# Performance work log

Measured on AMD Instinct MI355X. Metric: run time of the kernel, lower is better.

The kernel has to match this reference:

```python
import jax, jax.numpy as jnp
import numpy as np

DIM = 1024
N_HEADS = 16
MLP_DIM = 4096
DEPTH = 6
HEAD_DIM = DIM // N_HEADS
SCALE = DIM ** -0.5  # module uses full dim (self.dim_heads = dim), NOT head_dim
EPS = 1e-5


def setup_inputs() -> dict:
    key = jax.random.key(0)
    ks = jax.random.split(key, 12)
    s = lambda k, shape, fan: jax.random.normal(k, shape, jnp.float32) * (fan ** -0.5)
    return {
        "x": jax.random.normal(ks[0], (8, 1024, DIM), jnp.float32),
        "Wq": s(ks[1], (DIM, DIM), DIM), "bq": jnp.zeros((DIM,), jnp.float32),
        "Wk": s(ks[2], (DIM, DIM), DIM), "bk": jnp.zeros((DIM,), jnp.float32),
        "Wv": s(ks[3], (DIM, DIM), DIM), "bv": jnp.zeros((DIM,), jnp.float32),
        "W1": s(ks[4], (DIM, MLP_DIM), DIM), "b1": jnp.zeros((MLP_DIM,), jnp.float32),
        "W2": s(ks[5], (MLP_DIM, DIM), MLP_DIM), "b2": jnp.zeros((DIM,), jnp.float32),
        "gamma": jnp.ones((DIM,), jnp.float32),
        "beta": jnp.zeros((DIM,), jnp.float32),
    }


def _layernorm(x, gamma, beta):
    mu = jnp.mean(x, axis=-1, keepdims=True)
    var = jnp.mean(jnp.square(x - mu), axis=-1, keepdims=True)
    return (x - mu) * jax.lax.rsqrt(var + EPS) * gamma + beta


def _attention(x, Wq, bq, Wk, bk, Wv, bv):
    b, n, _ = x.shape
    split = lambda t: t.reshape(b, n, N_HEADS, HEAD_DIM).transpose(0, 2, 1, 3)  # b h n d
    q = split(x @ Wq + bq)
    k = split(x @ Wk + bk)
    v = split(x @ Wv + bv)
    logit = jnp.einsum('bhnd,bhmd->bhnm', q, k) * SCALE
    attn = jax.nn.softmax(logit, axis=-1)
    out = jnp.einsum('bhnm,bhmd->bhnd', attn, v)
    return out.transpose(0, 2, 1, 3).reshape(b, n, DIM)


def reference(x, Wq, bq, Wk, bk, Wv, bv, W1, b1, W2, b2, gamma, beta):
    # Same single attention + MLP modules (shared weights) applied `depth` times.
    for _ in range(DEPTH):
        x = _attention(_layernorm(x, gamma, beta), Wq, bq, Wk, bk, Wv, bv) + x
        h = _layernorm(x, gamma, beta)
        x = (jax.nn.gelu(h @ W1 + b1, approximate=False) @ W2 + b2) + x
    return x
```

## Files before the change

### kernel.cpp

```cpp
#include <hip/hip_runtime.h>
#include <cstdint>
#include <cmath>

typedef short bf16x8 __attribute__((ext_vector_type(8)));
typedef float f32x4 __attribute__((ext_vector_type(4)));

#define AS_GLOBAL(p) (const __attribute__((address_space(1))) void*)(p)
#define AS_LDS(p)    (__attribute__((address_space(3))) void*)(p)

#define QSCALE 0.04508422002778f

__device__ inline float b2f(unsigned short u) {
    union { unsigned int i; float f; } c; c.i = ((unsigned int)u) << 16; return c.f;
}
__device__ inline unsigned short f2b(float f) {
    return (unsigned short)((__float_as_uint(f) + 0x8000u) >> 16);
}
__device__ inline unsigned cvt_pk_bf16u(float lo, float hi) {
    unsigned r;
    asm("v_cvt_pk_bf16_f32 %0, %1, %2" : "=v"(r) : "v"(lo), "v"(hi));
    return r;
}
__device__ inline float fast_gelu(float x) {
    float arg = -x * (2.30223674f + 0.10294946f * x * x);
    float t = exp2f(arg);
    return x * __builtin_amdgcn_rcpf(1.f + t);
}

__device__ inline bf16x8 ldsfrag(const unsigned short* SM, int base_sh, int r, int lc) {
    return *(const bf16x8*)((const char*)SM + base_sh * 2 + r * 128 + ((lc ^ (r & 7)) << 4));
}

__global__ __launch_bounds__(256) void transpose_f32_to_bf16(
    const float* __restrict__ W, unsigned short* __restrict__ Wt, int K, int N)
{
    __shared__ unsigned short sh[32][33];
    int n0 = blockIdx.x * 32;
    int k0 = blockIdx.y * 32;
    int tr = threadIdx.x >> 5;
    int tc = threadIdx.x & 31;
#pragma unroll
    for (int i = 0; i < 4; i++)
        sh[tr + i * 8][tc] = f2b(W[(size_t)(k0 + tr + i * 8) * N + n0 + tc]);
    __syncthreads();
#pragma unroll
    for (int i = 0; i < 4; i++)
        Wt[(size_t)(n0 + tr + i * 8) * K + k0 + tc] = sh[tc][tr + i * 8];
}

__global__ __launch_bounds__(256) void concat_bias(const float* __restrict__ bq,
                                                   const float* __restrict__ bk,
                                                   float* __restrict__ bqk)
{
    int i = blockIdx.x * 256 + threadIdx.x;
    bqk[i] = (i < 1024) ? bq[i] : bk[i - 1024];
}

__global__ __launch_bounds__(256) void layernorm_k(
    const float* __restrict__ x, const float* __restrict__ gamma,
    const float* __restrict__ beta, unsigned short* __restrict__ out)
{
    int row = blockIdx.x;
    int t = threadIdx.x;
    f32x4 v = *(const f32x4*)(x + (size_t)row * 1024 + t * 4);
    float s  = v[0] + v[1] + v[2] + v[3];
    float s2 = v[0]*v[0] + v[1]*v[1] + v[2]*v[2] + v[3]*v[3];
#pragma unroll
    for (int off = 32; off >= 1; off >>= 1) {
        s  += __shfl_xor(s,  off);
        s2 += __shfl_xor(s2, off);
    }
    __shared__ float red[8];
    int w = t >> 6;
    if ((t & 63) == 0) { red[w] = s; red[4 + w] = s2; }
    __syncthreads();
    s  = red[0] + red[1] + red[2] + red[3];
    s2 = red[4] + red[5] + red[6] + red[7];
    float mu  = s * (1.f / 1024.f);
    float var = s2 * (1.f / 1024.f) - mu * mu;
    float rs  = rsqrtf(var + 1e-5f);
    int c = t * 4;
    f32x4 g = *(const f32x4*)(gamma + c);
    f32x4 be = *(const f32x4*)(beta + c);
    unsigned int lo, hi;
    {
        float o0 = (v[0] - mu) * rs * g[0] + be[0];
        float o1 = (v[1] - mu) * rs * g[1] + be[1];
        float o2 = (v[2] - mu) * rs * g[2] + be[2];
        float o3 = (v[3] - mu) * rs * g[3] + be[3];
        lo = (unsigned)f2b(o0) | ((unsigned)f2b(o1) << 16);
        hi = (unsigned)f2b(o2) | ((unsigned)f2b(o3) << 16);
    }
    uint2 pk; pk.x = lo; pk.y = hi;
    *(uint2*)(out + (size_t)row * 1024 + c) = pk;
}

template<int MODE, int NBNL, int BN, int SMALLM = 0>
__global__ __launch_bounds__(512, 2) void gemm256(
    const unsigned short* __restrict__ A,
    const unsigned short* __restrict__ Bt,
    const float* __restrict__ bias,
    const float* __restrict__ resid,
    void* __restrict__ outp,
    int M, int N, int K)
{
    constexpr int NFR = BN / 64;
    constexpr int WGN = BN / 64;
    constexpr int WM  = 2 * WGN;
    constexpr int HM  = WM / 2;
    extern __shared__ unsigned short LDS[];

    const int t   = threadIdx.x;
    const int bi  = blockIdx.x;
    const int xcd = bi & 7;
    const int j   = bi >> 3;
    int m_idx, n_idx;
    if (SMALLM) {
        m_idx = j >> 3;
        n_idx = xcd * 8 + (j & 7);
    } else {
        const int mper = M >> 11;
        m_idx = xcd * mper + (j >> NBNL);
        n_idx = j & ((1 << NBNL) - 1);
    }
    const int m0 = m_idx * 256;
    const int n0 = n_idx * BN;

    const int w    = t >> 6;
    const int lane = t & 63;
    const int l15  = lane & 15;
    const int q    = lane >> 4;
    const int wmb  = (w / WGN) * (WM * 16);
    const int wnb  = (w % WGN) * 64;
    const int xsw  = (l15 & 7) << 4;

    const int trow = t >> 3;
    const int csrc = ((t & 7) ^ (trow & 7)) << 3;
    const unsigned short* As0 = A  + (size_t)(m0 + trow) * K + csrc;
    const unsigned short* Bs0 = Bt + (size_t)(n0 + trow) * K + csrc;

    f32x4 acc[WM][4];
#pragma unroll
    for (int i = 0; i < WM; i++)
#pragma unroll
        for (int n = 0; n < 4; n++) acc[i][n] = (f32x4)0.f;

    auto STAGEP = [&](int Tn, int part) {
        const int bsel = Tn & 1;
        const size_t kk = (size_t)Tn << 6;
        if (part < 2) {
#pragma unroll
            for (int la = part * 2; la < part * 2 + 2; la++)
                __builtin_amdgcn_global_load_lds(
                    AS_GLOBAL(As0 + (size_t)la * 64 * K + kk),
                    AS_LDS(LDS + bsel * 16384 + la * 4096 + w * 512), 16, 0, 0);
        } else {
#pragma unroll
            for (int lb = (part - 2) * 2; lb < (part - 2) * 2 + 2; lb++)
                if (lb < NFR)
                    __builtin_amdgcn_global_load_lds(
                        AS_GLOBAL(Bs0 + (size_t)lb * 64 * K + kk),
                        AS_LDS(LDS + 32768 + bsel * (BN * 64) + lb * 4096 + w * 512), 16, 0, 0);
        }
    };
    auto RDAF = [&](const char* Ab, int ks, int mh, bf16x8* dst) {
        const int colx = ((ks * 64 + q * 16) ^ xsw);
#pragma unroll
        for (int m4 = 0; m4 < HM; m4++)
            dst[m4] = *(const bf16x8*)(Ab + (wmb + (mh * HM + m4) * 16 + l15) * 128 + colx);
    };
    auto RDBV = [&](const char* Bb, int ks, bf16x8* dst) {
        const int colx = ((ks * 64 + q * 16) ^ xsw);
#pragma unroll
        for (int ni = 0; ni < 4; ni++)
            dst[ni] = *(const bf16x8*)(Bb + (wnb + ni * 16 + l15) * 128 + colx);
    };
    auto MM = [&](int mh, bf16x8* afs, bf16x8* bvs) {
        __builtin_amdgcn_s_setprio(1);
#pragma unroll
        for (int m4 = 0; m4 < HM; m4++)
#pragma unroll
            for (int ni = 0; ni < 4; ni++)
                acc[mh * HM + m4][ni] = __builtin_amdgcn_mfma_f32_16x16x32_bf16(
                    afs[m4], bvs[ni], acc[mh * HM + m4][ni], 0, 0, 0);
        __builtin_amdgcn_s_setprio(0);
        __builtin_amdgcn_sched_barrier(0);
    };

    bf16x8 afA[HM], afB[HM], bvA[4], bvB[4];

    STAGEP(0, 0); STAGEP(0, 1); STAGEP(0, 2); STAGEP(0, 3);
    asm volatile("s_waitcnt vmcnt(0)" ::: "memory");
    __builtin_amdgcn_s_barrier();
    RDBV((const char*)LDS + 65536, 0, bvA);
    RDAF((const char*)LDS, 0, 0, afA);

    const int NT = K >> 6;
    for (int T = 0; T < NT; T++) {
        const char* Ab = (const char*)LDS + (T & 1) * 32768;
        const char* Bb = (const char*)LDS + 65536 + (T & 1) * (BN * 128);
        const bool pf = (T + 1 < NT);

        RDAF(Ab, 0, 1, afB);
        if (pf) STAGEP(T + 1, 0);
        __builtin_amdgcn_s_barrier();
        if (BN == 256) asm volatile("s_waitcnt lgkmcnt(4)" ::: "memory");
        else           asm volatile("s_waitcnt lgkmcnt(2)" ::: "memory");
        __builtin_amdgcn_sched_barrier(0);
        MM(0, afA, bvA);

        RDBV(Bb, 1, bvB);
        RDAF(Ab, 1, 0, afA);
        if (pf) STAGEP(T + 1, 1);
        __builtin_amdgcn_s_barrier();
        if (BN == 256) asm volatile("s_waitcnt lgkmcnt(8)" ::: "memory");
        else           asm volatile("s_waitcnt lgkmcnt(6)" ::: "memory");
        __builtin_amdgcn_sched_barrier(0);
        MM(1, afB, bvA);

        RDAF(Ab, 1, 1, afB);
        if (pf) STAGEP(T + 1, 2);
        __builtin_amdgcn_s_barrier();
        if (BN == 256) asm volatile("s_waitcnt lgkmcnt(4)" ::: "memory");
        else           asm volatile("s_waitcnt lgkmcnt(2)" ::: "memory");
        __builtin_amdgcn_sched_barrier(0);
        MM(0, afA, bvB);

        if (pf) STAGEP(T + 1, 3);
        __builtin_amdgcn_s_barrier();
        asm volatile("s_waitcnt lgkmcnt(0)" ::: "memory");
        __builtin_amdgcn_sched_barrier(0);
        MM(1, afB, bvB);

        asm volatile("s_waitcnt vmcnt(0)" ::: "memory");
        __builtin_amdgcn_s_barrier();
        if (pf) {
            const char* AbN = (const char*)LDS + ((T + 1) & 1) * 32768;
            const char* BbN = (const char*)LDS + 65536 + ((T + 1) & 1) * (BN * 128);
            RDBV(BbN, 0, bvA);
            RDAF(AbN, 0, 0, afA);
        }
    }

    const float qsc = (MODE == 5 && n0 < 1024) ? QSCALE : 1.f;
#pragma unroll
    for (int mi = 0; mi < WM; mi++) {
        const int gr0 = m0 + wmb + mi * 16 + q * 4;
#pragma unroll
        for (int ni = 0; ni < 4; ni++) {
            const int gc = n0 + wnb + ni * 16 + l15;
            const float bv = (MODE == 3) ? 0.f : bias[gc];
#pragma unroll
            for (int r = 0; r < 4; r++) {
                const int gr = gr0 + r;
                float v = acc[mi][ni][r] + ((MODE == 3) ? bias[gr] : bv);
                if (MODE == 1) {
                    ((unsigned short*)outp)[(size_t)gr * N + gc] = f2b(fast_gelu(v));
                } else if (MODE == 2) {
                    ((float*)outp)[(size_t)gr * N + gc] = resid[(size_t)gr * N + gc] + v;
                } else if (MODE == 3) {
                    ((unsigned short*)outp)[(size_t)gr * N + gc] = f2b(v);
                } else {
                    ((unsigned short*)outp)[(size_t)gr * N + gc] = f2b(v * qsc);
                }
            }
        }
    }
}

__global__ __launch_bounds__(256, 4) void attn_k(
    const unsigned short* __restrict__ qkb,
    const unsigned short* __restrict__ vtb,
    const float* __restrict__ xres,
    float* __restrict__ xout)
{
    __shared__ unsigned short SM[20480];

    const int t    = threadIdx.x;
    const int blk  = blockIdx.x;
    const int qt   = blk >> 7;
    const int bh   = blk & 127;
    const int h    = bh & 15;
    const int b    = bh >> 4;
    const int w    = t >> 6;
    const int lane = t & 63;
    const int l15  = lane & 15;
    const int quad = lane >> 4;
    const int wrow = w * 32;

    const int sr  = t >> 3;
    const int slc = (t & 7) ^ (sr & 7);
    const unsigned short* Qsrc = qkb + ((size_t)(b * 1024 + qt * 128 + sr)) * 2048 + h * 64 + slc * 8;
    const unsigned short* Ksrc = qkb + ((size_t)(b * 1024 + sr)) * 2048 + 1024 + h * 64 + slc * 8;
    const unsigned short* Vsrc = vtb + ((size_t)(h * 64 + sr)) * 8192 + (size_t)b * 1024 + slc * 8;

    auto GLL = [&](const unsigned short* g, int sh) {
        __builtin_amdgcn_global_load_lds(AS_GLOBAL(g), AS_LDS(SM + sh + w * 512), 16, 0, 0);
    };

#pragma unroll
    for (int c = 0; c < 4; c++) GLL(Qsrc + (size_t)c * 32 * 2048, c * 2048);
#pragma unroll
    for (int c = 0; c < 2; c++) GLL(Ksrc + (size_t)c * 32 * 2048, 8192 + c * 2048);
#pragma unroll
    for (int c = 0; c < 2; c++) GLL(Ksrc + (size_t)(64 + c * 32) * 2048, 12288 + c * 2048);
#pragma unroll
    for (int c = 0; c < 2; c++) GLL(Vsrc + (size_t)c * 32 * 8192, 16384 + c * 2048);
    asm volatile("s_waitcnt vmcnt(0)" ::: "memory");
    __builtin_amdgcn_s_barrier();

    bf16x8 qf[2][2];
#pragma unroll
    for (int nt2 = 0; nt2 < 2; nt2++)
#pragma unroll
        for (int kd = 0; kd < 2; kd++)
            qf[nt2][kd] = ldsfrag(SM, 0, wrow + nt2 * 16 + l15, kd * 4 + quad);

    const bf16x8 onesv = (bf16x8)(short)0x3F80;
    float m_s[2] = { -1e30f, -1e30f };
    f32x4 l_acc[2] = { (f32x4)0.f, (f32x4)0.f };
    f32x4 O[2][4];
#pragma unroll
    for (int nt2 = 0; nt2 < 2; nt2++)
#pragma unroll
        for (int dt = 0; dt < 4; dt++) O[nt2][dt] = (f32x4)0.f;

    for (int kt = 0; kt < 16; ++kt) {
        const int cur = kt & 1;
        if (kt > 0) {
            const unsigned short* vs = Vsrc + kt * 64;
            GLL(vs, 16384);
            GLL(vs + (size_t)32 * 8192, 16384 + 2048);
        }

        f32x4 s[4][2];
#pragma unroll
        for (int mt = 0; mt < 4; mt++) {
            bf16x8 kf0 = ldsfrag(SM, 8192 + cur * 4096, mt * 16 + l15, quad);
            bf16x8 kf1 = ldsfrag(SM, 8192 + cur * 4096, mt * 16 + l15, 4 + quad);
#pragma unroll
            for (int nt2 = 0; nt2 < 2; nt2++) {
                f32x4 a = (f32x4)0.f;
                a = __builtin_amdgcn_mfma_f32_16x16x32_bf16(kf0, qf[nt2][0], a, 0, 0, 0);
                a = __builtin_amdgcn_mfma_f32_16x16x32_bf16(kf1, qf[nt2][1], a, 0, 0, 0);
                s[mt][nt2] = a;
            }
        }

#pragma unroll
        for (int nt2 = 0; nt2 < 2; nt2++) {
            float tm = -1e30f;
#pragma unroll
            for (int mt = 0; mt < 4; mt++) {
                f32x4 sv = s[mt][nt2];
                tm = fmaxf(tm, fmaxf(fmaxf(sv[0], sv[1]), fmaxf(sv[2], sv[3])));
            }
            tm = fmaxf(tm, __shfl_xor(tm, 16));
            tm = fmaxf(tm, __shfl_xor(tm, 32));
            if (!__all(tm <= m_s[nt2])) {
                float nm    = fmaxf(m_s[nt2], tm);
                float alpha = exp2f(m_s[nt2] - nm);
                m_s[nt2] = nm;
                l_acc[nt2] *= alpha;
#pragma unroll
                for (int dt = 0; dt < 4; dt++) O[nt2][dt] *= alpha;
            }
            const float nm = m_s[nt2];
            const int r = wrow + nt2 * 16 + l15;
#pragma unroll
            for (int mt = 0; mt < 4; mt++) {
                float p0 = exp2f(s[mt][nt2][0] - nm);
                float p1 = exp2f(s[mt][nt2][1] - nm);
                float p2 = exp2f(s[mt][nt2][2] - nm);
                float p3 = exp2f(s[mt][nt2][3] - nm);
                uint2 pk;
                pk.x = cvt_pk_bf16u(p0, p1);
                pk.y = cvt_pk_bf16u(p2, p3);
                *(uint2*)((char*)SM + r * 128 + (((2 * mt + (quad >> 1)) ^ (r & 7)) << 4)
                          + (quad & 1) * 8) = pk;
            }
        }

        asm volatile("s_waitcnt vmcnt(0)" ::: "memory");
        __builtin_amdgcn_s_barrier();

        if (kt + 2 < 16) {
            const unsigned short* ks = Ksrc + (size_t)(kt + 2) * 64 * 2048;
            GLL(ks, 8192 + cur * 4096);
            GLL(ks + (size_t)32 * 2048, 8192 + cur * 4096 + 2048);
        }

        bf16x8 pf[2][2];
#pragma unroll
        for (int nt2 = 0; nt2 < 2; nt2++)
#pragma unroll
            for (int kc = 0; kc < 2; kc++)
                pf[nt2][kc] = ldsfrag(SM, 0, wrow + nt2 * 16 + l15, kc * 4 + quad);
#pragma unroll
        for (int nt2 = 0; nt2 < 2; nt2++) {
            l_acc[nt2] = __builtin_amdgcn_mfma_f32_16x16x32_bf16(onesv, pf[nt2][0], l_acc[nt2], 0, 0, 0);
            l_acc[nt2] = __builtin_amdgcn_mfma_f32_16x16x32_bf16(onesv, pf[nt2][1], l_acc[nt2], 0, 0, 0);
        }
#pragma unroll
        for (int dt = 0; dt < 4; dt++) {
            bf16x8 vf0 = ldsfrag(SM, 16384, dt * 16 + l15, quad);
            bf16x8 vf1 = ldsfrag(SM, 16384, dt * 16 + l15, 4 + quad);
#pragma unroll
            for (int nt2 = 0; nt2 < 2; nt2++) {
                O[nt2][dt] = __builtin_amdgcn_mfma_f32_16x16x32_bf16(vf0, pf[nt2][0], O[nt2][dt], 0, 0, 0);
                O[nt2][dt] = __builtin_amdgcn_mfma_f32_16x16x32_bf16(vf1, pf[nt2][1], O[nt2][dt], 0, 0, 0);
            }
        }

        __builtin_amdgcn_s_barrier();
    }

    {
        float inv0 = 1.f / l_acc[0][0], inv1 = 1.f / l_acc[1][0];
#pragma unroll
        for (int nt2 = 0; nt2 < 2; nt2++) {
            float inv = (nt2 == 0) ? inv0 : inv1;
            const int r = wrow + nt2 * 16 + l15;
#pragma unroll
            for (int dt = 0; dt < 4; dt++) {
                uint2 pk;
                pk.x = cvt_pk_bf16u(O[nt2][dt][0] * inv, O[nt2][dt][1] * inv);
                pk.y = cvt_pk_bf16u(O[nt2][dt][2] * inv, O[nt2][dt][3] * inv);
                *(uint2*)((char*)SM + 16384 + r * 128 + (((2 * dt + (quad >> 1)) ^ (r & 7)) << 4)
                          + (quad & 1) * 8) = pk;
            }
        }
    }
    __syncthreads();
    {
        int r0 = t >> 2;
        int qc = t & 3;
#pragma unroll
        for (int half = 0; half < 2; half++) {
            int r = r0 + half * 64;
            size_t off = ((size_t)(b * 1024 + qt * 128 + r)) * 1024 + h * 64 + qc * 16;
            const float* xrp = xres + off;
            float* xwp = xout + off;
#pragma unroll
            for (int jj = 0; jj < 2; jj++) {
                uint4 u = *(const uint4*)((const char*)SM + 16384 + r * 128
                                          + (((qc * 2 + jj) ^ (r & 7)) << 4));
                f32x4 xv0 = *(const f32x4*)(xrp + jj * 8);
                f32x4 xv1 = *(const f32x4*)(xrp + jj * 8 + 4);
                xv0[0] += b2f((unsigned short)(u.x & 0xffff));
                xv0[1] += b2f((unsigned short)(u.x >> 16));
                xv0[2] += b2f((unsigned short)(u.y & 0xffff));
                xv0[3] += b2f((unsigned short)(u.y >> 16));
                xv1[0] += b2f((unsigned short)(u.z & 0xffff));
                xv1[1] += b2f((unsigned short)(u.z >> 16));
                xv1[2] += b2f((unsigned short)(u.w & 0xffff));
                xv1[3] += b2f((unsigned short)(u.w >> 16));
                *(f32x4*)(xwp + jj * 8)     = xv0;
                *(f32x4*)(xwp + jj * 8 + 4) = xv1;
            }
        }
    }
}

extern "C" void kernel_launch(void* const* d_in, const int* in_sizes, int n_in,
                              void* d_out, int out_size, void* d_ws, size_t ws_size,
                              hipStream_t stream)
{
    (void)in_sizes; (void)n_in; (void)out_size; (void)ws_size;
    const float* x_in  = (const float*)d_in[0];
    const float* Wq    = (const float*)d_in[1];
    const float* bq    = (const float*)d_in[2];
    const float* Wk    = (const float*)d_in[3];
    const float* bk    = (const float*)d_in[4];
    const float* Wv    = (const float*)d_in[5];
    const float* bv    = (const float*)d_in[6];
    const float* W1    = (const float*)d_in[7];
    const float* b1    = (const float*)d_in[8];
    const float* W2    = (const float*)d_in[9];
    const float* b2    = (const float*)d_in[10];
    const float* gamma = (const float*)d_in[11];
    const float* beta  = (const float*)d_in[12];

    char* base = (char*)d_ws;
    float*          xf   = (float*)(base);
    unsigned short* xn   = (unsigned short*)(base + 33554432);
    unsigned short* qkb  = (unsigned short*)(base + 50331648);
    unsigned short* vtb  = (unsigned short*)(base + 50331648 + 33554432);
    unsigned short* h1   = (unsigned short*)(base + 50331648);
    char* wbase = base + 50331648 + 67108864;
    unsigned short* WqkT = (unsigned short*)(wbase);
    unsigned short* WvT  = (unsigned short*)(wbase + 4194304);
    unsigned short* W1T  = (unsigned short*)(wbase + 6291456);
    unsigned short* W2T  = (unsigned short*)(wbase + 14680064);
    float*          bqk  = (float*)(wbase + 23068672);

    transpose_f32_to_bf16<<<dim3(32, 32),  256, 0, stream>>>(Wq, WqkT, 1024, 1024);
    transpose_f32_to_bf16<<<dim3(32, 32),  256, 0, stream>>>(Wk, WqkT + 1048576, 1024, 1024);
    transpose_f32_to_bf16<<<dim3(32, 32),  256, 0, stream>>>(Wv, WvT, 1024, 1024);
    transpose_f32_to_bf16<<<dim3(128, 32), 256, 0, stream>>>(W1, W1T, 1024, 4096);
    transpose_f32_to_bf16<<<dim3(32, 128), 256, 0, stream>>>(W2, W2T, 4096, 1024);
    concat_bias<<<8, 256, 0, stream>>>(bq, bk, bqk);

    for (int layer = 0; layer < 6; ++layer) {
        const float* xcur = (layer == 0) ? x_in : xf;
        layernorm_k<<<8192, 256, 0, stream>>>(xcur, gamma, beta, xn);
        gemm256<5, 3, 256><<<256, 512, 131072, stream>>>(xn, WqkT, bqk, nullptr, qkb, 8192, 2048, 1024);
        gemm256<3, 0, 128, 1><<<256, 512, 98304, stream>>>(WvT, xn, bv, nullptr, vtb, 1024, 8192, 1024);
        attn_k<<<1024, 256, 0, stream>>>(qkb, vtb, xcur, xf);
        layernorm_k<<<8192, 256, 0, stream>>>(xf, gamma, beta, xn);
        gemm256<1, 4, 256><<<512, 512, 131072, stream>>>(xn, W1T, b1, nullptr, h1, 8192, 4096, 1024);
        float* mout = (layer == 5) ? (float*)d_out : xf;
        gemm256<2, 3, 128><<<256, 512, 98304, stream>>>(h1, W2T, b2, xf, mout, 8192, 1024, 4096);
    }
}
```

Before: 1.877 ms.

## Reorder BN=256 GEMM prefetch stages and change tile rasterization to M-fastest

After: 1.893 ms. Within noise of the previous version (+0.9%).

```diff
diff --git a/kernel.cpp b/kernel.cpp
--- a/kernel.cpp
+++ b/kernel.cpp
@@ -120,8 +120,8 @@
         n_idx = xcd * 8 + (j & 7);
     } else {
         const int mper = M >> 11;
-        m_idx = xcd * mper + (j >> NBNL);
-        n_idx = j & ((1 << NBNL) - 1);
+        m_idx = xcd * mper + (j & (mper - 1));
+        n_idx = j >> __builtin_ctz(mper);
     }
     const int m0 = m_idx * 256;
     const int n0 = n_idx * BN;
@@ -145,23 +145,19 @@
 #pragma unroll
         for (int n = 0; n < 4; n++) acc[i][n] = (f32x4)0.f;
 
-    auto STAGEP = [&](int Tn, int part) {
+    auto SA1 = [&](int Tn, int la) {
         const int bsel = Tn & 1;
         const size_t kk = (size_t)Tn << 6;
-        if (part < 2) {
-#pragma unroll
-            for (int la = part * 2; la < part * 2 + 2; la++)
-                __builtin_amdgcn_global_load_lds(
-                    AS_GLOBAL(As0 + (size_t)la * 64 * K + kk),
-                    AS_LDS(LDS + bsel * 16384 + la * 4096 + w * 512), 16, 0, 0);
-        } else {
-#pragma unroll
-            for (int lb = (part - 2) * 2; lb < (part - 2) * 2 + 2; lb++)
-                if (lb < NFR)
-                    __builtin_amdgcn_global_load_lds(
-                        AS_GLOBAL(Bs0 + (size_t)lb * 64 * K + kk),
-                        AS_LDS(LDS + 32768 + bsel * (BN * 64) + lb * 4096 + w * 512), 16, 0, 0);
-        }
+        __builtin_amdgcn_global_load_lds(
+            AS_GLOBAL(As0 + (size_t)la * 64 * K + kk),
+            AS_LDS(LDS + bsel * 16384 + la * 4096 + w * 512), 16, 0, 0);
+    };
+    auto SB1 = [&](int Tn, int lb) {
+        const int bsel = Tn & 1;
+        const size_t kk = (size_t)Tn << 6;
+        __builtin_amdgcn_global_load_lds(
+            AS_GLOBAL(Bs0 + (size_t)lb * 64 * K + kk),
+            AS_LDS(LDS + 32768 + bsel * (BN * 64) + lb * 4096 + w * 512), 16, 0, 0);
     };
     auto RDAF = [&](const char* Ab, int ks, int mh, bf16x8* dst) {
         const int colx = ((ks * 64 + q * 16) ^ xsw);
@@ -188,57 +184,112 @@
     };
 
     bf16x8 afA[HM], afB[HM], bvA[4], bvB[4];
-
-    STAGEP(0, 0); STAGEP(0, 1); STAGEP(0, 2); STAGEP(0, 3);
-    asm volatile("s_waitcnt vmcnt(0)" ::: "memory");
-    __builtin_amdgcn_s_barrier();
-    RDBV((const char*)LDS + 65536, 0, bvA);
-    RDAF((const char*)LDS, 0, 0, afA);
-
     const int NT = K >> 6;
-    for (int T = 0; T < NT; T++) {
-        const char* Ab = (const char*)LDS + (T & 1) * 32768;
-        const char* Bb = (const char*)LDS + 65536 + (T & 1) * (BN * 128);
-        const bool pf = (T + 1 < NT);
-
-        RDAF(Ab, 0, 1, afB);
-        if (pf) STAGEP(T + 1, 0);
-        __builtin_amdgcn_s_barrier();
-        if (BN == 256) asm volatile("s_waitcnt lgkmcnt(4)" ::: "memory");
-        else           asm volatile("s_waitcnt lgkmcnt(2)" ::: "memory");
-        __builtin_amdgcn_sched_barrier(0);
-        MM(0, afA, bvA);
-
-        RDBV(Bb, 1, bvB);
-        RDAF(Ab, 1, 0, afA);
-        if (pf) STAGEP(T + 1, 1);
-        __builtin_amdgcn_s_barrier();
-        if (BN == 256) asm volatile("s_waitcnt lgkmcnt(8)" ::: "memory");
-        else           asm volatile("s_waitcnt lgkmcnt(6)" ::: "memory");
-        __builtin_amdgcn_sched_barrier(0);
-        MM(1, afB, bvA);
-
-        RDAF(Ab, 1, 1, afB);
-        if (pf) STAGEP(T + 1, 2);
-        __builtin_amdgcn_s_barrier();
-        if (BN == 256) asm volatile("s_waitcnt lgkmcnt(4)" ::: "memory");
-        else           asm volatile("s_waitcnt lgkmcnt(2)" ::: "memory");
-        __builtin_amdgcn_sched_barrier(0);
-        MM(0, afA, bvB);
-
-        if (pf) STAGEP(T + 1, 3);
-        __builtin_amdgcn_s_barrier();
-        asm volatile("s_waitcnt lgkmcnt(0)" ::: "memory");
-        __builtin_amdgcn_sched_barrier(0);
-        MM(1, afB, bvB);
-
+
+    if constexpr (BN == 256) {
+#pragma unroll
+        for (int g = 0; g < 4; g++) { SB1(0, g); SA1(0, g); }
         asm volatile("s_waitcnt vmcnt(0)" ::: "memory");
         __builtin_amdgcn_s_barrier();
-        if (pf) {
-            const char* AbN = (const char*)LDS + ((T + 1) & 1) * 32768;
-            const char* BbN = (const char*)LDS + 65536 + ((T + 1) & 1) * (BN * 128);
-            RDBV(BbN, 0, bvA);
-            RDAF(AbN, 0, 0, afA);
+        RDBV((const char*)LDS + 65536, 0, bvA);
+        RDAF((const char*)LDS, 0, 0, afA);
+
+        for (int T = 0; T < NT; T++) {
+            const char* Ab = (const char*)LDS + (T & 1) * 32768;
+            const char* Bb = (const char*)LDS + 65536 + (T & 1) * (BN * 128);
+            const bool pf = (T + 1 < NT);
+
+            if (pf) { SB1(T + 1, 0); SB1(T + 1, 1);
+                      asm volatile("s_waitcnt vmcnt(2)" ::: "memory"); }
+            else    { asm volatile("s_waitcnt vmcnt(0)" ::: "memory"); }
+            __builtin_amdgcn_s_barrier();
+            RDAF(Ab, 0, 1, afB);
+            asm volatile("s_waitcnt lgkmcnt(4)" ::: "memory");
+            __builtin_amdgcn_sched_barrier(0);
+            MM(0, afA, bvA);
+
+            if (pf) { SB1(T + 1, 2); SB1(T + 1, 3); }
+            __builtin_amdgcn_s_barrier();
+            RDBV(Bb, 1, bvB);
+            RDAF(Ab, 1, 0, afA);
+            asm volatile("s_waitcnt lgkmcnt(8)" ::: "memory");
+            __builtin_amdgcn_sched_barrier(0);
+            MM(1, afB, bvA);
+
+            if (pf) { SA1(T + 1, 0); SA1(T + 1, 2); }
+            __builtin_amdgcn_s_barrier();
+            RDAF(Ab, 1, 1, afB);
+            asm volatile("s_waitcnt lgkmcnt(4)" ::: "memory");
+            __builtin_amdgcn_sched_barrier(0);
+            MM(0, afA, bvB);
+
+            if (pf) { SA1(T + 1, 1); SA1(T + 1, 3); }
+            __builtin_amdgcn_s_barrier();
+            asm volatile("s_waitcnt lgkmcnt(0)" ::: "memory");
+            __builtin_amdgcn_sched_barrier(0);
+            MM(1, afB, bvB);
+
+            if (pf) {
+                asm volatile("s_waitcnt vmcnt(2)" ::: "memory");
+                __builtin_amdgcn_s_barrier();
+                const char* AbN = (const char*)LDS + ((T + 1) & 1) * 32768;
+                const char* BbN = (const char*)LDS + 65536 + ((T + 1) & 1) * (BN * 128);
+                RDBV(BbN, 0, bvA);
+                RDAF(AbN, 0, 0, afA);
+            }
+        }
+    } else {
+        auto STAGEP = [&](int Tn, int part) {
+            if (part < 2) { SA1(Tn, part * 2); SA1(Tn, part * 2 + 1); }
+            else if (part == 2) { SB1(Tn, 0); SB1(Tn, 1); }
+        };
+        STAGEP(0, 0); STAGEP(0, 1); STAGEP(0, 2); STAGEP(0, 3);
+        asm volatile("s_waitcnt vmcnt(0)" ::: "memory");
+        __builtin_amdgcn_s_barrier();
+        RDBV((const char*)LDS + 65536, 0, bvA);
+        RDAF((const char*)LDS, 0, 0, afA);
+
+        for (int T = 0; T < NT; T++) {
+            const char* Ab = (const char*)LDS + (T & 1) * 32768;
+            const char* Bb = (const char*)LDS + 65536 + (T & 1) * (BN * 128);
+            const bool pf = (T + 1 < NT);
+
+            RDAF(Ab, 0, 1, afB);
+            if (pf) STAGEP(T + 1, 0);
+            __builtin_amdgcn_s_barrier();
+            asm volatile("s_waitcnt lgkmcnt(2)" ::: "memory");
+            __builtin_amdgcn_sched_barrier(0);
+            MM(0, afA, bvA);
+
+            RDBV(Bb, 1, bvB);
+            RDAF(Ab, 1, 0, afA);
+            if (pf) STAGEP(T + 1, 1);
+            __builtin_amdgcn_s_barrier();
+            asm volatile("s_waitcnt lgkmcnt(6)" ::: "memory");
+            __builtin_amdgcn_sched_barrier(0);
+            MM(1, afB, bvA);
+
+            RDAF(Ab, 1, 1, afB);
+            if (pf) STAGEP(T + 1, 2);
+            __builtin_amdgcn_s_barrier();
+            asm volatile("s_waitcnt lgkmcnt(2)" ::: "memory");
+            __builtin_amdgcn_sched_barrier(0);
+            MM(0, afA, bvB);
+
+            if (pf) STAGEP(T + 1, 3);
+            __builtin_amdgcn_s_barrier();
+            asm volatile("s_waitcnt lgkmcnt(0)" ::: "memory");
+            __builtin_amdgcn_sched_barrier(0);
+            MM(1, afB, bvB);
+
+            asm volatile("s_waitcnt vmcnt(0)" ::: "memory");
+            __builtin_amdgcn_s_barrier();
+            if (pf) {
+                const char* AbN = (const char*)LDS + ((T + 1) & 1) * 32768;
+                const char* BbN = (const char*)LDS + 65536 + ((T + 1) & 1) * (BN * 128);
+                RDBV(BbN, 0, bvA);
+                RDAF(AbN, 0, 0, afA);
+            }
         }
     }
 
```
